# Performance work log

Measured on AMD Instinct MI355X. Metric: run time of the kernel, lower is better.

Reference implementation:

```python
import jax, jax.numpy as jnp
import numpy as np

QUALITY = 95
X_MIN, X_MAX = 0.0, 1.0

# JPEG Annex K base quantization tables
_LUMA = np.array([
    [16, 11, 10, 16, 24, 40, 51, 61],
    [12, 12, 14, 19, 26, 58, 60, 55],
    [14, 13, 16, 24, 40, 57, 69, 56],
    [14, 17, 22, 29, 51, 87, 80, 62],
    [18, 22, 37, 56, 68, 109, 103, 77],
    [24, 35, 55, 64, 81, 104, 113, 92],
    [49, 64, 78, 87, 103, 121, 120, 101],
    [72, 92, 95, 98, 112, 100, 103, 99]], dtype=np.float32)
_CHROMA = np.array([
    [17, 18, 24, 47, 99, 99, 99, 99],
    [18, 21, 26, 66, 99, 99, 99, 99],
    [24, 26, 56, 99, 99, 99, 99, 99],
    [47, 66, 99, 99, 99, 99, 99, 99],
    [99, 99, 99, 99, 99, 99, 99, 99],
    [99, 99, 99, 99, 99, 99, 99, 99],
    [99, 99, 99, 99, 99, 99, 99, 99],
    [99, 99, 99, 99, 99, 99, 99, 99]], dtype=np.float32)

def _qtable(base, quality):
    # libjpeg quality scaling (quality >= 50 branch)
    scale = 5000.0 / quality if quality < 50 else 200.0 - 2.0 * quality
    return np.clip(np.floor((base * scale + 50.0) / 100.0), 1.0, 255.0).astype(np.float32)

_QL = jnp.asarray(_qtable(_LUMA, QUALITY))
_QC = jnp.asarray(_qtable(_CHROMA, QUALITY))

# Orthonormal 8x8 DCT-II matrix
_k = np.arange(8)
_D = np.sqrt(2.0 / 8.0) * np.cos((2 * _k[None, :] + 1) * _k[:, None] * np.pi / 16.0)
_D[0, :] /= np.sqrt(2.0)
_D = jnp.asarray(_D.astype(np.float32))

def _jpeg_channel(ch, table):
    """8x8 block DCT -> quantize(round) -> dequantize -> IDCT. ch: [B,H,W] level-shifted."""
    B, H, W = ch.shape
    xb = ch.reshape(B, H // 8, 8, W // 8, 8)
    coef = jnp.einsum('ki,bhiwj,lj->bhkwl', _D, xb, _D)
    t = table[None, None, :, None, :]
    deq = jnp.round(coef / t) * t
    rec = jnp.einsum('ki,bhkwl,lj->bhiwj', _D, deq, _D)
    return rec.reshape(B, H, W)

def _jpeg_roundtrip(x255):
    """x255: [B,H,W,3] float values in [0,255]. Simulates JPEG encode+decode (4:2:0)."""
    r, g, b = x255[..., 0], x255[..., 1], x255[..., 2]
    # JFIF RGB -> YCbCr
    y = 0.299 * r + 0.587 * g + 0.114 * b
    cb = -0.168736 * r - 0.331264 * g + 0.5 * b + 128.0
    cr = 0.5 * r - 0.418688 * g - 0.081312 * b + 128.0
    # Luma at full resolution
    y2 = _jpeg_channel(y - 128.0, _QL) + 128.0
    # Chroma: 2x2 average downsample (4:2:0), codec, nearest upsample
    def down(c):
        B, H, W = c.shape
        return c.reshape(B, H // 2, 2, W // 2, 2).mean(axis=(2, 4))
    def up(c):
        return jnp.repeat(jnp.repeat(c, 2, axis=1), 2, axis=2)
    cb2 = up(_jpeg_channel(down(cb) - 128.0, _QC) + 128.0)
    cr2 = up(_jpeg_channel(down(cr) - 128.0, _QC) + 128.0)
    # YCbCr -> RGB
    r2 = y2 + 1.402 * (cr2 - 128.0)
    g2 = y2 - 0.344136 * (cb2 - 128.0) - 0.714136 * (cr2 - 128.0)
    b2 = y2 + 1.772 * (cb2 - 128.0)
    rgb = jnp.stack([r2, g2, b2], axis=-1)
    return jnp.round(jnp.clip(rgb, 0.0, 255.0))  # decoded uint8 values


def setup_inputs() -> dict:
    key = jax.random.key(0)
    x = jax.random.uniform(key, (32, 512, 512, 3), dtype=jnp.float32)
    return {"x": x}


def reference(x):
    # inputs -> uint8 pixel values (tf.cast truncation; values are >= 0)
    x255 = jnp.clip(jnp.floor((x - X_MIN) / ((X_MAX - X_MIN) / 255.0)), 0.0, 255.0)
    dec = _jpeg_roundtrip(x255)
    # back to input range/dtype
    return dec / (255.0 / (X_MAX - X_MIN)) + X_MIN
```

## Files before the change

### kernel.cpp

```cpp
#include <hip/hip_runtime.h>
#include <cstddef>

static constexpr float D8[8][8] = {
  { 0.35355339059327373f, 0.35355339059327373f, 0.35355339059327373f, 0.35355339059327373f,
    0.35355339059327373f, 0.35355339059327373f, 0.35355339059327373f, 0.35355339059327373f},
  { 0.4903926402016152f,  0.4157348061512726f,  0.27778511650980114f, 0.09754516100806417f,
   -0.09754516100806417f,-0.27778511650980114f,-0.4157348061512726f, -0.4903926402016152f},
  { 0.46193976625564337f, 0.19134171618254492f,-0.19134171618254492f,-0.46193976625564337f,
   -0.46193976625564337f,-0.19134171618254492f, 0.19134171618254492f, 0.46193976625564337f},
  { 0.4157348061512726f, -0.09754516100806417f,-0.4903926402016152f, -0.27778511650980114f,
    0.27778511650980114f, 0.4903926402016152f,  0.09754516100806417f,-0.4157348061512726f},
  { 0.35355339059327373f,-0.35355339059327373f,-0.35355339059327373f, 0.35355339059327373f,
    0.35355339059327373f,-0.35355339059327373f,-0.35355339059327373f, 0.35355339059327373f},
  { 0.27778511650980114f,-0.4903926402016152f,  0.09754516100806417f, 0.4157348061512726f,
   -0.4157348061512726f, -0.09754516100806417f, 0.4903926402016152f, -0.27778511650980114f},
  { 0.19134171618254492f,-0.46193976625564337f, 0.46193976625564337f,-0.19134171618254492f,
   -0.19134171618254492f, 0.46193976625564337f,-0.46193976625564337f, 0.19134171618254492f},
  { 0.09754516100806417f,-0.27778511650980114f, 0.4157348061512726f, -0.4903926402016152f,
    0.4903926402016152f, -0.4157348061512726f,  0.27778511650980114f,-0.09754516100806417f},
};

static constexpr float QLt[8][8] = {
  {2,1,1,2,2,4,5,6},
  {1,1,1,2,3,6,6,6},
  {1,1,2,2,4,6,7,6},
  {1,2,2,3,5,9,8,6},
  {2,2,4,6,7,11,10,8},
  {2,4,6,6,8,10,11,9},
  {5,6,8,9,10,12,12,10},
  {7,9,10,10,11,10,10,10},
};
static constexpr float QCt[8][8] = {
  {2,2,2,5,10,10,10,10},
  {2,2,3,7,10,10,10,10},
  {2,3,6,10,10,10,10,10},
  {5,7,10,10,10,10,10,10},
  {10,10,10,10,10,10,10,10},
  {10,10,10,10,10,10,10,10},
  {10,10,10,10,10,10,10,10},
  {10,10,10,10,10,10,10,10},
};

struct F2 { float q, r; };
struct QTab { F2 v[8][8]; };
static constexpr QTab mkq(const float (&b)[8][8]) {
  QTab t{};
  for (int i = 0; i < 8; ++i)
    for (int j = 0; j < 8; ++j) { t.v[i][j].q = b[i][j]; t.v[i][j].r = 1.0f / b[i][j]; }
  return t;
}
static constexpr QTab QLp = mkq(QLt);
static constexpr QTab QCp = mkq(QCt);

__device__ __forceinline__ void dct8(const float x[8], float u[8]) {
  #pragma unroll
  for (int k = 0; k < 8; ++k) {
    float a = D8[k][0] * x[0];
    #pragma unroll
    for (int j = 1; j < 8; ++j) a += D8[k][j] * x[j];
    u[k] = a;
  }
}
__device__ __forceinline__ void idct8(const float x[8], float u[8]) {
  #pragma unroll
  for (int j = 0; j < 8; ++j) {
    float a = x[0] * D8[0][j];
    #pragma unroll
    for (int m = 1; m < 8; ++m) a += x[m] * D8[m][j];
    u[j] = a;
  }
}

__device__ __forceinline__ float to255(float x) {
  const float c255 = (float)(1.0 / 255.0);
  float y  = x * 255.0f;
  float fl = floorf(y);
  float fr = y - fl;
  if (__builtin_expect(fr < 2e-4f || fr > 1.0f - 2e-4f, 0)) {
    fl = floorf(x / c255);
  }
  return fminf(fmaxf(fl, 0.0f), 255.0f);
}

__device__ __forceinline__ float quant_rt(float u, F2 qp) {
  float tq = u * qp.r;
  float n  = rintf(tq);
  float d  = fabsf(tq - n);
  if (__builtin_expect(d > 0.499f, 0)) {
    n = rintf(u / qp.q);
  }
  return n * qp.q;
}

__global__ __launch_bounds__(256) void jpeg_rt(const float* __restrict__ in,
                                               float* __restrict__ out)
{
  __shared__ __align__(16) float U[3264];
  __shared__ __align__(16) float V[3264];

  const int t   = threadIdx.x;
  const int tx  = blockIdx.x;
  const int ty  = blockIdx.y;
  const int img = blockIdx.z;

  const int pr = t >> 5;
  const int pc = t & 31;

  float* Yp  = U;
  float* Cbp = U + 2112;
  float* Crp = U + 2656;

  {
    float yv[2][4], cbv[2][4], crv[2][4];
    #pragma unroll
    for (int rr = 0; rr < 2; ++rr) {
      const size_t grow = (size_t)img * 512 + (size_t)(ty*16 + 2*pr + rr);
      const float* rp = in + (grow*512 + (size_t)(tx*128 + 4*pc))*3;
      float4 A = ((const float4*)rp)[0];
      float4 Bq = ((const float4*)rp)[1];
      float4 Cq = ((const float4*)rp)[2];
      float px[12] = {A.x,A.y,A.z,A.w,Bq.x,Bq.y,Bq.z,Bq.w,Cq.x,Cq.y,Cq.z,Cq.w};
      #pragma unroll
      for (int p = 0; p < 4; ++p) {
        float r = to255(px[3*p+0]);
        float g = to255(px[3*p+1]);
        float b = to255(px[3*p+2]);
        float y  =  0.299f*r + 0.587f*g + 0.114f*b;
        float cb = -0.168736f*r - 0.331264f*g + 0.5f*b + 128.0f;
        float cr =  0.5f*r - 0.418688f*g - 0.081312f*b + 128.0f;
        yv[rr][p]  = y - 128.0f;
        cbv[rr][p] = cb;
        crv[rr][p] = cr;
      }
    }
    *(float4*)&Yp[(2*pr+0)*132 + 4*pc] = make_float4(yv[0][0],yv[0][1],yv[0][2],yv[0][3]);
    *(float4*)&Yp[(2*pr+1)*132 + 4*pc] = make_float4(yv[1][0],yv[1][1],yv[1][2],yv[1][3]);
    float cb0 = ((cbv[0][0]+cbv[0][1]) + (cbv[1][0]+cbv[1][1]))*0.25f - 128.0f;
    float cb1 = ((cbv[0][2]+cbv[0][3]) + (cbv[1][2]+cbv[1][3]))*0.25f - 128.0f;
    float cr0 = ((crv[0][0]+crv[0][1]) + (crv[1][0]+crv[1][1]))*0.25f - 128.0f;
    float cr1 = ((crv[0][2]+crv[0][3]) + (crv[1][2]+crv[1][3]))*0.25f - 128.0f;
    *(float2*)&Cbp[pr*68 + 2*pc] = make_float2(cb0, cb1);
    *(float2*)&Crp[pr*68 + 2*pc] = make_float2(cr0, cr1);
  }
  __syncthreads();

  #pragma unroll
  for (int task = t; task < 384; task += 256) {
    const int tb = task >> 3, i = task & 7;
    const float* src;
    if (tb < 32)      src = Yp  + (size_t)((tb>>4)*8 + i)*132 + (tb&15)*8;
    else if (tb < 40) src = Cbp + i*68 + (tb-32)*8;
    else              src = Crp + i*68 + (tb-40)*8;
    float xr[8], u[8];
    *(float4*)&xr[0] = *(const float4*)&src[0];
    *(float4*)&xr[4] = *(const float4*)&src[4];
    dct8(xr, u);
    *(float4*)&V[tb*68 + i*8 + 0] = make_float4(u[0],u[1],u[2],u[3]);
    *(float4*)&V[tb*68 + i*8 + 4] = make_float4(u[4],u[5],u[6],u[7]);
  }
  __syncthreads();

  #pragma unroll
  for (int task = t; task < 384; task += 256) {
    const int tb = task >> 3, kk = task & 7;
    float s[8], u[8], v[8];
    #pragma unroll
    for (int i = 0; i < 8; ++i) s[i] = V[tb*68 + i*8 + kk];
    dct8(s, u);
    if (tb < 32) {
      #pragma unroll
      for (int m = 0; m < 8; ++m) u[m] = quant_rt(u[m], QLp.v[m][kk]);
    } else {
      #pragma unroll
      for (int m = 0; m < 8; ++m) u[m] = quant_rt(u[m], QCp.v[m][kk]);
    }
    idct8(u, v);
    *(float4*)&U[tb*68 + kk*8 + 0] = make_float4(v[0],v[1],v[2],v[3]);
    *(float4*)&U[tb*68 + kk*8 + 4] = make_float4(v[4],v[5],v[6],v[7]);
  }
  __syncthreads();

  float* Yr  = V;
  float* Cbr = V + 2112;
  float* Crr = V + 2656;
  #pragma unroll
  for (int task = t; task < 384; task += 256) {
    const int tb = task >> 3, j = task & 7;
    float w[8], z[8];
    #pragma unroll
    for (int m = 0; m < 8; ++m) w[m] = U[tb*68 + m*8 + j];
    idct8(w, z);
    float* dst;
    if (tb < 32)      dst = Yr  + (size_t)((tb>>4)*8 + j)*132 + (tb&15)*8;
    else if (tb < 40) dst = Cbr + j*68 + (tb-32)*8;
    else              dst = Crr + j*68 + (tb-40)*8;
    *(float4*)&dst[0] = make_float4(z[0],z[1],z[2],z[3]);
    *(float4*)&dst[4] = make_float4(z[4],z[5],z[6],z[7]);
  }
  __syncthreads();

  {
    const float c255 = (float)(1.0 / 255.0);
    float y0[4], y1[4];
    *(float4*)y0 = *(const float4*)&Yr[(2*pr+0)*132 + 4*pc];
    *(float4*)y1 = *(const float4*)&Yr[(2*pr+1)*132 + 4*pc];
    float2 cbp2 = *(const float2*)&Cbr[pr*68 + 2*pc];
    float2 crp2 = *(const float2*)&Crr[pr*68 + 2*pc];
    float cbq[2] = {cbp2.x, cbp2.y};
    float crq[2] = {crp2.x, crp2.y};
    #pragma unroll
    for (int rr = 0; rr < 2; ++rr) {
      float ov[12];
      #pragma unroll
      for (int p = 0; p < 4; ++p) {
        float y2  = (rr ? y1[p] : y0[p]) + 128.0f;
        float cb2 = cbq[p>>1] + 128.0f;
        float cr2 = crq[p>>1] + 128.0f;
        float r2 = y2 + 1.402f*(cr2 - 128.0f);
        float g2 = y2 - 0.344136f*(cb2 - 128.0f) - 0.714136f*(cr2 - 128.0f);
        float b2 = y2 + 1.772f*(cb2 - 128.0f);
        ov[3*p+0] = rintf(fminf(fmaxf(r2, 0.0f), 255.0f)) * c255;
        ov[3*p+1] = rintf(fminf(fmaxf(g2, 0.0f), 255.0f)) * c255;
        ov[3*p+2] = rintf(fminf(fmaxf(b2, 0.0f), 255.0f)) * c255;
      }
      const size_t grow = (size_t)img * 512 + (size_t)(ty*16 + 2*pr + rr);
      float* op = out + (grow*512 + (size_t)(tx*128 + 4*pc))*3;
      ((float4*)op)[0] = make_float4(ov[0],ov[1],ov[2],ov[3]);
      ((float4*)op)[1] = make_float4(ov[4],ov[5],ov[6],ov[7]);
      ((float4*)op)[2] = make_float4(ov[8],ov[9],ov[10],ov[11]);
    }
  }
}

extern "C" void kernel_launch(void* const* d_in, const int* in_sizes, int n_in,
                              void* d_out, int out_size, void* d_ws, size_t ws_size,
                              hipStream_t stream) {
  (void)in_sizes; (void)n_in; (void)d_ws; (void)ws_size; (void)out_size;
  const float* x = (const float*)d_in[0];
  float* out = (float*)d_out;
  dim3 grid(4, 32, 32);
  jpeg_rt<<<grid, dim3(256), 0, stream>>>(x, out);
}
```

Baseline: 188.0 us.

## Give each wavefront its own tile and remove block-wide barriers

```diff
diff --git a/kernel.cpp b/kernel.cpp
--- a/kernel.cpp
+++ b/kernel.cpp
@@ -92,39 +92,45 @@
   return n * qp.q;
 }
 
-__global__ __launch_bounds__(256) void jpeg_rt(const float* __restrict__ in,
+__global__ __launch_bounds__(128) void jpeg_rt(const float* __restrict__ in,
                                                float* __restrict__ out)
 {
-  __shared__ __align__(16) float U[3264];
-  __shared__ __align__(16) float V[3264];
+  __shared__ __align__(16) float LDSB[2 * 1792];
 
   const int t   = threadIdx.x;
+  const int w   = t >> 6;
+  const int l   = t & 63;
   const int tx  = blockIdx.x;
   const int ty  = blockIdx.y;
   const int img = blockIdx.z;
 
-  const int pr = t >> 5;
-  const int pc = t & 31;
-
-  float* Yp  = U;
-  float* Cbp = U + 2112;
-  float* Crp = U + 2656;
+  float* A = LDSB + w * 1792;
+  float* B = A + 896;
+
+  const int pr = l >> 3;
+  const int pc = l & 7;
+  const int colbase = tx*64 + w*32 + 4*pc;
 
   {
+    const size_t r0 = (size_t)img * 512 + (size_t)(ty*16 + 2*pr);
+    const float* rp0 = in + (r0*512 + colbase)*3;
+    const float* rp1 = rp0 + 512*3;
+    float4 L0 = ((const float4*)rp0)[0];
+    float4 L1 = ((const float4*)rp0)[1];
+    float4 L2 = ((const float4*)rp0)[2];
+    float4 L3 = ((const float4*)rp1)[0];
+    float4 L4 = ((const float4*)rp1)[1];
+    float4 L5 = ((const float4*)rp1)[2];
+    float px[2][12] = {{L0.x,L0.y,L0.z,L0.w,L1.x,L1.y,L1.z,L1.w,L2.x,L2.y,L2.z,L2.w},
+                       {L3.x,L3.y,L3.z,L3.w,L4.x,L4.y,L4.z,L4.w,L5.x,L5.y,L5.z,L5.w}};
     float yv[2][4], cbv[2][4], crv[2][4];
     #pragma unroll
     for (int rr = 0; rr < 2; ++rr) {
-      const size_t grow = (size_t)img * 512 + (size_t)(ty*16 + 2*pr + rr);
-      const float* rp = in + (grow*512 + (size_t)(tx*128 + 4*pc))*3;
-      float4 A = ((const float4*)rp)[0];
-      float4 Bq = ((const float4*)rp)[1];
-      float4 Cq = ((const float4*)rp)[2];
-      float px[12] = {A.x,A.y,A.z,A.w,Bq.x,Bq.y,Bq.z,Bq.w,Cq.x,Cq.y,Cq.z,Cq.w};
       #pragma unroll
       for (int p = 0; p < 4; ++p) {
-        float r = to255(px[3*p+0]);
-        float g = to255(px[3*p+1]);
-        float b = to255(px[3*p+2]);
+        float r = to255(px[rr][3*p+0]);
+        float g = to255(px[rr][3*p+1]);
+        float b = to255(px[rr][3*p+2]);
         float y  =  0.299f*r + 0.587f*g + 0.114f*b;
         float cb = -0.168736f*r - 0.331264f*g + 0.5f*b + 128.0f;
         float cr =  0.5f*r - 0.418688f*g - 0.081312f*b + 128.0f;
@@ -133,79 +139,81 @@
         crv[rr][p] = cr;
       }
     }
-    *(float4*)&Yp[(2*pr+0)*132 + 4*pc] = make_float4(yv[0][0],yv[0][1],yv[0][2],yv[0][3]);
-    *(float4*)&Yp[(2*pr+1)*132 + 4*pc] = make_float4(yv[1][0],yv[1][1],yv[1][2],yv[1][3]);
+    *(float4*)&A[(2*pr+0)*36 + 4*pc] = make_float4(yv[0][0],yv[0][1],yv[0][2],yv[0][3]);
+    *(float4*)&A[(2*pr+1)*36 + 4*pc] = make_float4(yv[1][0],yv[1][1],yv[1][2],yv[1][3]);
     float cb0 = ((cbv[0][0]+cbv[0][1]) + (cbv[1][0]+cbv[1][1]))*0.25f - 128.0f;
     float cb1 = ((cbv[0][2]+cbv[0][3]) + (cbv[1][2]+cbv[1][3]))*0.25f - 128.0f;
     float cr0 = ((crv[0][0]+crv[0][1]) + (crv[1][0]+crv[1][1]))*0.25f - 128.0f;
     float cr1 = ((crv[0][2]+crv[0][3]) + (crv[1][2]+crv[1][3]))*0.25f - 128.0f;
-    *(float2*)&Cbp[pr*68 + 2*pc] = make_float2(cb0, cb1);
-    *(float2*)&Crp[pr*68 + 2*pc] = make_float2(cr0, cr1);
-  }
-  __syncthreads();
-
-  #pragma unroll
-  for (int task = t; task < 384; task += 256) {
-    const int tb = task >> 3, i = task & 7;
-    const float* src;
-    if (tb < 32)      src = Yp  + (size_t)((tb>>4)*8 + i)*132 + (tb&15)*8;
-    else if (tb < 40) src = Cbp + i*68 + (tb-32)*8;
-    else              src = Crp + i*68 + (tb-40)*8;
-    float xr[8], u[8];
-    *(float4*)&xr[0] = *(const float4*)&src[0];
-    *(float4*)&xr[4] = *(const float4*)&src[4];
-    dct8(xr, u);
-    *(float4*)&V[tb*68 + i*8 + 0] = make_float4(u[0],u[1],u[2],u[3]);
-    *(float4*)&V[tb*68 + i*8 + 4] = make_float4(u[4],u[5],u[6],u[7]);
-  }
-  __syncthreads();
-
-  #pragma unroll
-  for (int task = t; task < 384; task += 256) {
-    const int tb = task >> 3, kk = task & 7;
-    float s[8], u[8], v[8];
-    #pragma unroll
-    for (int i = 0; i < 8; ++i) s[i] = V[tb*68 + i*8 + kk];
-    dct8(s, u);
-    if (tb < 32) {
-      #pragma unroll
-      for (int m = 0; m < 8; ++m) u[m] = quant_rt(u[m], QLp.v[m][kk]);
-    } else {
-      #pragma unroll
-      for (int m = 0; m < 8; ++m) u[m] = quant_rt(u[m], QCp.v[m][kk]);
-    }
-    idct8(u, v);
-    *(float4*)&U[tb*68 + kk*8 + 0] = make_float4(v[0],v[1],v[2],v[3]);
-    *(float4*)&U[tb*68 + kk*8 + 4] = make_float4(v[4],v[5],v[6],v[7]);
-  }
-  __syncthreads();
-
-  float* Yr  = V;
-  float* Cbr = V + 2112;
-  float* Crr = V + 2656;
-  #pragma unroll
-  for (int task = t; task < 384; task += 256) {
-    const int tb = task >> 3, j = task & 7;
-    float w[8], z[8];
-    #pragma unroll
-    for (int m = 0; m < 8; ++m) w[m] = U[tb*68 + m*8 + j];
-    idct8(w, z);
-    float* dst;
-    if (tb < 32)      dst = Yr  + (size_t)((tb>>4)*8 + j)*132 + (tb&15)*8;
-    else if (tb < 40) dst = Cbr + j*68 + (tb-32)*8;
-    else              dst = Crr + j*68 + (tb-40)*8;
-    *(float4*)&dst[0] = make_float4(z[0],z[1],z[2],z[3]);
-    *(float4*)&dst[4] = make_float4(z[4],z[5],z[6],z[7]);
-  }
-  __syncthreads();
+    *(float2*)&A[576 + pr*20 + 2*pc] = make_float2(cb0, cb1);
+    *(float2*)&A[736 + pr*20 + 2*pc] = make_float2(cr0, cr1);
+  }
+
+  auto planeAddr = [](int tb, int i) -> int {
+    if (tb < 8)  return ((tb >> 2)*8 + i)*36 + (tb & 3)*8;
+    if (tb < 10) return 576 + i*20 + (tb - 8)*8;
+    return 736 + i*20 + (tb - 10)*8;
+  };
+
+  #pragma unroll
+  for (int iter = 0; iter < 2; ++iter) {
+    const int task = iter*64 + l;
+    if (task < 96) {
+      const int tb = task >> 3, i = task & 7;
+      const float* src = A + planeAddr(tb, i);
+      float xr[8], u[8];
+      *(float4*)&xr[0] = *(const float4*)&src[0];
+      *(float4*)&xr[4] = *(const float4*)&src[4];
+      dct8(xr, u);
+      *(float4*)&B[tb*68 + i*8 + 0] = make_float4(u[0],u[1],u[2],u[3]);
+      *(float4*)&B[tb*68 + i*8 + 4] = make_float4(u[4],u[5],u[6],u[7]);
+    }
+  }
+
+  #pragma unroll
+  for (int iter = 0; iter < 2; ++iter) {
+    const int task = iter*64 + l;
+    if (task < 96) {
+      const int tb = task >> 3, kk = task & 7;
+      float s[8], u[8], v[8];
+      #pragma unroll
+      for (int i = 0; i < 8; ++i) s[i] = B[tb*68 + i*8 + kk];
+      dct8(s, u);
+      if (tb < 8) {
+        #pragma unroll
+        for (int m = 0; m < 8; ++m) u[m] = quant_rt(u[m], QLp.v[m][kk]);
+      } else {
+        #pragma unroll
+        for (int m = 0; m < 8; ++m) u[m] = quant_rt(u[m], QCp.v[m][kk]);
+      }
+      idct8(u, v);
+      *(float4*)&A[tb*68 + kk*8 + 0] = make_float4(v[0],v[1],v[2],v[3]);
+      *(float4*)&A[tb*68 + kk*8 + 4] = make_float4(v[4],v[5],v[6],v[7]);
+    }
+  }
+
+  #pragma unroll
+  for (int iter = 0; iter < 2; ++iter) {
+    const int task = iter*64 + l;
+    if (task < 96) {
+      const int tb = task >> 3, j = task & 7;
+      float wv[8], z[8];
+      #pragma unroll
+      for (int m = 0; m < 8; ++m) wv[m] = A[tb*68 + m*8 + j];
+      idct8(wv, z);
+      float* dst = B + planeAddr(tb, j);
+      *(float4*)&dst[0] = make_float4(z[0],z[1],z[2],z[3]);
+      *(float4*)&dst[4] = make_float4(z[4],z[5],z[6],z[7]);
+    }
+  }
 
   {
     const float c255 = (float)(1.0 / 255.0);
     float y0[4], y1[4];
-    *(float4*)y0 = *(const float4*)&Yr[(2*pr+0)*132 + 4*pc];
-    *(float4*)y1 = *(const float4*)&Yr[(2*pr+1)*132 + 4*pc];
-    float2 cbp2 = *(const float2*)&Cbr[pr*68 + 2*pc];
-    float2 crp2 = *(const float2*)&Crr[pr*68 + 2*pc];
+    *(float4*)y0 = *(const float4*)&B[(2*pr+0)*36 + 4*pc];
+    *(float4*)y1 = *(const float4*)&B[(2*pr+1)*36 + 4*pc];
+    float2 cbp2 = *(const float2*)&B[576 + pr*20 + 2*pc];
+    float2 crp2 = *(const float2*)&B[736 + pr*20 + 2*pc];
     float cbq[2] = {cbp2.x, cbp2.y};
     float crq[2] = {crp2.x, crp2.y};
     #pragma unroll
@@ -224,7 +232,7 @@
         ov[3*p+2] = rintf(fminf(fmaxf(b2, 0.0f), 255.0f)) * c255;
       }
       const size_t grow = (size_t)img * 512 + (size_t)(ty*16 + 2*pr + rr);
-      float* op = out + (grow*512 + (size_t)(tx*128 + 4*pc))*3;
+      float* op = out + (grow*512 + colbase)*3;
       ((float4*)op)[0] = make_float4(ov[0],ov[1],ov[2],ov[3]);
       ((float4*)op)[1] = make_float4(ov[4],ov[5],ov[6],ov[7]);
       ((float4*)op)[2] = make_float4(ov[8],ov[9],ov[10],ov[11]);
@@ -238,6 +246,6 @@
   (void)in_sizes; (void)n_in; (void)d_ws; (void)ws_size; (void)out_size;
   const float* x = (const float*)d_in[0];
   float* out = (float*)d_out;
-  dim3 grid(4, 32, 32);
-  jpeg_rt<<<grid, dim3(256), 0, stream>>>(x, out);
-}
+  dim3 grid(8, 32, 32);
+  jpeg_rt<<<grid, dim3(128), 0, stream>>>(x, out);
+}
```

After: 188.9 us. Within noise of the previous version (+0.5%).
